# Kernel tuning notes

Measured on AMD Instinct MI355X. Metric: run time of the kernel, lower is better.

The kernel has to match this reference:

```python
import jax, jax.numpy as jnp
import numpy as np

B, T, N, F_IN, F_OUT = 8, 16, 512, 128, 64
NEG_INF = -9e15


def setup_inputs() -> dict:
    key = jax.random.key(0)
    k1, k2, k3, k4, k5 = jax.random.split(key, 5)
    x = jax.random.normal(k1, (B, T, N, F_IN), dtype=jnp.float32)
    # nn.Linear weights: FC_W [out, in], FC_a [1, 2*out], no bias
    W = jax.random.normal(k2, (F_OUT, F_IN), dtype=jnp.float32) * 0.05
    a = jax.random.normal(k3, (1, 2 * F_OUT), dtype=jnp.float32) * 0.05
    adj = jax.random.randint(k4, (N, N), 0, 2, dtype=jnp.int32)
    adj_we = jax.random.uniform(k5, (N, N), dtype=jnp.float32)
    return {"x": x, "W": W, "a": a, "adj": adj, "adj_we": adj_we}


def reference(x, W, a, adj, adj_we):
    fout = W.shape[0]
    # h = FC_W(input): [B,T,N,Fout]
    h = jnp.einsum("btnf,of->btno", x, W)
    # Additive GAT score decomposition: e[i,j] = LeakyReLU(a1.h_i + a2.h_j)
    # (equivalent to FC_a(cat([h_i, h_j])) without materializing [B,T,N,N,2F])
    a1 = a[0, :fout]
    a2 = a[0, fout:]
    src = jnp.einsum("btno,o->btn", h, a1)  # contribution of node i (repeated rows)
    dst = jnp.einsum("btno,o->btn", h, a2)  # contribution of node j (tiled rows)
    e = jax.nn.leaky_relu(src[..., :, None] + dst[..., None, :], negative_slope=0.01)
    # mask where adj <= 0, scale by edge weights, softmax over neighbors (dim=3)
    att = jnp.where(adj > 0, e, NEG_INF)
    att = att * adj_we
    att = jax.nn.softmax(att, axis=-1)
    # h_prime = attention @ h : [B,T,N,N] @ [B,T,N,Fout]
    return jnp.einsum("btij,btjo->btio", att, h)
```

## Files before the change

### kernel.cpp

```cpp
#include <hip/hip_runtime.h>
#include <hip/hip_bf16.h>

#define BTOT 128
#define NN   512
#define FIN  128
#define FOUT 64

typedef __attribute__((ext_vector_type(8))) short bf16x8;
typedef __attribute__((ext_vector_type(4))) float f32x4;

static __device__ inline ushort f2bf(float f) {
    __hip_bfloat16 h = __float2bfloat16(f);
    return *(ushort*)&h;
}
static __device__ inline float bf2f(ushort u) {
    uint v = (uint)u << 16;
    return __uint_as_float(v);
}

__global__ void k_prep(const float* __restrict__ W, const int* __restrict__ adj,
                       const float* __restrict__ we, ushort* __restrict__ Whi,
                       ushort* __restrict__ Wlo, ushort* __restrict__ cds) {
    int b = blockIdx.x;
    if (b >= 256) {
        int i = (b - 256) * 256 + threadIdx.x;
        float w = W[i];
        ushort hi = f2bf(w);
        Whi[i] = hi;
        Wlo[i] = f2bf(w - bf2f(hi));
        return;
    }
    int i = (b * 256 + threadIdx.x) * 4;
    int4   a4 = *(const int4*)&adj[i];
    float4 w4 = *(const float4*)&we[i];
    ushort o[4];
#pragma unroll
    for (int e = 0; e < 4; ++e) {
        bool  cn = ((const int*)&a4)[e] > 0;
        float w  = ((const float*)&w4)[e];
        if (cn) {
            uint ub = __float_as_uint(w * 1.44269504f);
            uint t  = ub + 0xFFFFu + ((ub >> 17) & 1u);
            o[e] = (ushort)(((t >> 17) << 1) | 1u);
        } else {
            o[e] = (w > 0.f) ? (ushort)0 : (ushort)1;
        }
    }
    *(uint2*)&cds[i] = *(uint2*)&o[0];
}

__global__ void k_feat(const float* __restrict__ x, const ushort* __restrict__ Whi,
                       const ushort* __restrict__ Wlo, const float* __restrict__ a,
                       ushort* __restrict__ ht, float* __restrict__ srcv,
                       float* __restrict__ dstv) {
    const int t    = threadIdx.x;
    const int bid  = blockIdx.x;
    const int bt   = bid & 127;
    const int nt   = bid >> 7;
    const int wv   = t >> 6, lane = t & 63;
    const int r    = lane & 15;
    const int kc   = lane >> 4;
    const int n0   = nt * 64 + wv * 16;

    const float* xrow = x + ((long)bt * NN + n0 + r) * FIN;

    f32x4 acc[4] = {{0,0,0,0},{0,0,0,0},{0,0,0,0},{0,0,0,0}};

#pragma unroll
    for (int ks = 0; ks < 4; ++ks) {
        f32x4 xa = __builtin_nontemporal_load((const f32x4*)&xrow[ks * 32 + kc * 8]);
        f32x4 xb = __builtin_nontemporal_load((const f32x4*)&xrow[ks * 32 + kc * 8 + 4]);
        float xv[8] = {xa[0], xa[1], xa[2], xa[3], xb[0], xb[1], xb[2], xb[3]};
        bf16x8 Ahi, Alo;
#pragma unroll
        for (int e = 0; e < 8; ++e) {
            uint b = __float_as_uint(xv[e]);
            float hf = __uint_as_float(b & 0xFFFF0000u);
            Ahi[e] = (short)(b >> 16);
            float rr = xv[e] - hf;
            Alo[e] = (short)(__float_as_uint(rr) >> 16);
        }
#pragma unroll
        for (int g = 0; g < 4; ++g) {
            const int wo = (g * 16 + r) * FIN + ks * 32 + kc * 8;
            bf16x8 Bhi = *(const bf16x8*)&Whi[wo];
            bf16x8 Blo = *(const bf16x8*)&Wlo[wo];
            acc[g] = __builtin_amdgcn_mfma_f32_16x16x32_bf16(Ahi, Bhi, acc[g], 0, 0, 0);
            acc[g] = __builtin_amdgcn_mfma_f32_16x16x32_bf16(Alo, Bhi, acc[g], 0, 0, 0);
            acc[g] = __builtin_amdgcn_mfma_f32_16x16x32_bf16(Ahi, Blo, acc[g], 0, 0, 0);
        }
    }

    float a1g[4], a2g[4];
#pragma unroll
    for (int g = 0; g < 4; ++g) {
        a1g[g] = a[g * 16 + r];
        a2g[g] = a[FOUT + g * 16 + r];
    }
    f32x4 s1v = {0,0,0,0}, s2v = {0,0,0,0};
#pragma unroll
    for (int g = 0; g < 4; ++g)
#pragma unroll
        for (int reg = 0; reg < 4; ++reg) {
            s1v[reg] += acc[g][reg] * a1g[g];
            s2v[reg] += acc[g][reg] * a2g[g];
        }
#pragma unroll
    for (int off = 8; off; off >>= 1)
#pragma unroll
        for (int reg = 0; reg < 4; ++reg) {
            s1v[reg] += __shfl_down(s1v[reg], off, 16);
            s2v[reg] += __shfl_down(s2v[reg], off, 16);
        }
    if (r == 0) {
        float4 o1 = make_float4(s1v[0], s1v[1], s1v[2], s1v[3]);
        float4 o2 = make_float4(s2v[0], s2v[1], s2v[2], s2v[3]);
        *(float4*)&srcv[bt * NN + n0 + kc * 4] = o1;
        *(float4*)&dstv[bt * NN + n0 + kc * 4] = o2;
    }

#pragma unroll
    for (int g = 0; g < 4; ++g) {
        uint2 pk;
        pk.x = (uint)f2bf(acc[g][0]) | ((uint)f2bf(acc[g][1]) << 16);
        pk.y = (uint)f2bf(acc[g][2]) | ((uint)f2bf(acc[g][3]) << 16);
        *(uint2*)&ht[(long)bt * (FOUT * NN) + (g * 16 + r) * NN + n0 + kc * 4] = pk;
    }
}

static __device__ inline bf16x8 make_afrag(uint4 c, float4 d0, float4 d1, float si) {
    float dv[8] = {d0.x, d0.y, d0.z, d0.w, d1.x, d1.y, d1.z, d1.w};
    uint  cw[4] = {c.x, c.y, c.z, c.w};
    bf16x8 A;
#pragma unroll
    for (int q = 0; q < 4; ++q) {
        uint u = cw[q];
        float c0 = __uint_as_float((u << 16) & 0xFFFE0000u);
        float c1 = __uint_as_float(u & 0xFFFE0000u);
        float s0 = si + dv[2 * q],     lr0 = fmaxf(s0, 0.01f * s0);
        float s1 = si + dv[2 * q + 1], lr1 = fmaxf(s1, 0.01f * s1);
        float p0 = __builtin_amdgcn_exp2f(c0 * lr0);
        float p1 = __builtin_amdgcn_exp2f(c1 * lr1);
        p0 = (u & 1u)       ? p0 : 0.f;
        p1 = (u & 0x10000u) ? p1 : 0.f;
        A[2 * q]     = (short)(__float_as_uint(p0) >> 16);
        A[2 * q + 1] = (short)(__float_as_uint(p1) >> 16);
    }
    return A;
}

__global__ __launch_bounds__(256, 4)
void k_attn(const ushort* __restrict__ ht, const float* __restrict__ srcv,
            const float* __restrict__ dstv, const ushort* __restrict__ cds,
            float* __restrict__ out) {
    __shared__ ushort hs[64 * 256];
    __shared__ float dst_s[NN];

    const int t    = threadIdx.x;
    const int bid  = blockIdx.x;
    const int bt   = bid & 127;
    const int i0   = (bid >> 7) << 6;
    const int lane = t & 63;
    const int wv   = t >> 6;
    const int r16  = lane & 15;
    const int kq   = lane >> 4;
    const int koff = kq * 8;
    const int xr   = r16 & 7;

    const int ri = i0 + wv * 16 + r16;
    const float si = srcv[bt * NN + ri];
    const ushort* cdr = cds + ri * NN;
    const ushort* htb = ht + (long)bt * (FOUT * NN);

    for (int q = t; q < NN; q += 256) dst_s[q] = dstv[bt * NN + q];

    f32x4 acc0 = {0,0,0,0}, acc1 = {0,0,0,0}, acc2 = {0,0,0,0},
          acc3 = {0,0,0,0}, accd = {0,0,0,0};
    bf16x8 ones;
#pragma unroll
    for (int j = 0; j < 8; ++j) ones[j] = (short)0x3F80;

    for (int half = 0; half < 2; ++half) {
        __syncthreads();
#pragma unroll
        for (int q = 0; q < 8; ++q) {
            int idx = q * 256 + t;
            int o = idx >> 5, c8 = idx & 31;
            float4 v = *(const float4*)&htb[(o << 9) + (half << 8) + (c8 << 3)];
            *(float4*)&hs[(o << 8) + ((c8 ^ (o & 7)) << 3)] = v;
        }
        __syncthreads();

        const int jg = half * 256;
        uint4 cA = *(const uint4*)&cdr[jg + koff];
        uint4 cB = *(const uint4*)&cdr[jg + 32 + koff];

#pragma unroll
        for (int jtl = 0; jtl < 4; ++jtl) {
            const int jgc = jg + jtl * 64;
            uint4 nA = {0,0,0,0}, nB = {0,0,0,0};
            if (jtl < 3) {
                nA = *(const uint4*)&cdr[jgc + 64 + koff];
                nB = *(const uint4*)&cdr[jgc + 96 + koff];
            }
            float4 d00 = *(float4*)&dst_s[jgc + koff];
            float4 d01 = *(float4*)&dst_s[jgc + koff + 4];
            float4 d10 = *(float4*)&dst_s[jgc + 32 + koff];
            float4 d11 = *(float4*)&dst_s[jgc + 32 + koff + 4];

            bf16x8 A0 = make_afrag(cA, d00, d01, si);
            bf16x8 A1 = make_afrag(cB, d10, d11, si);

#pragma unroll
            for (int s2 = 0; s2 < 2; ++s2) {
                bf16x8 A = s2 ? A1 : A0;
                const int c8v = jtl * 8 + s2 * 4 + kq;
                const int cs  = (c8v ^ xr) << 3;
                bf16x8 b0 = *(bf16x8*)&hs[(( 0 + r16) << 8) + cs];
                bf16x8 b1 = *(bf16x8*)&hs[((16 + r16) << 8) + cs];
                bf16x8 b2 = *(bf16x8*)&hs[((32 + r16) << 8) + cs];
                bf16x8 b3 = *(bf16x8*)&hs[((48 + r16) << 8) + cs];
                acc0 = __builtin_amdgcn_mfma_f32_16x16x32_bf16(A, b0, acc0, 0, 0, 0);
                acc1 = __builtin_amdgcn_mfma_f32_16x16x32_bf16(A, b1, acc1, 0, 0, 0);
                acc2 = __builtin_amdgcn_mfma_f32_16x16x32_bf16(A, b2, acc2, 0, 0, 0);
                acc3 = __builtin_amdgcn_mfma_f32_16x16x32_bf16(A, b3, acc3, 0, 0, 0);
                accd = __builtin_amdgcn_mfma_f32_16x16x32_bf16(A, ones, accd, 0, 0, 0);
            }
            cA = nA; cB = nB;
        }
    }

    const int orow = wv * 16 + (lane >> 4) * 4;
    const int ocol = lane & 15;
    float* ob = out + ((long)bt * NN + i0) * FOUT;
#pragma unroll
    for (int reg = 0; reg < 4; ++reg) {
        float inv = 1.0f / accd[reg];
        __builtin_nontemporal_store(acc0[reg] * inv, &ob[(orow + reg) * FOUT +  0 + ocol]);
        __builtin_nontemporal_store(acc1[reg] * inv, &ob[(orow + reg) * FOUT + 16 + ocol]);
        __builtin_nontemporal_store(acc2[reg] * inv, &ob[(orow + reg) * FOUT + 32 + ocol]);
        __builtin_nontemporal_store(acc3[reg] * inv, &ob[(orow + reg) * FOUT + 48 + ocol]);
    }
}

extern "C" void kernel_launch(void* const* d_in, const int* in_sizes, int n_in,
                              void* d_out, int out_size, void* d_ws, size_t ws_size,
                              hipStream_t stream) {
    const float* x      = (const float*)d_in[0];
    const float* W      = (const float*)d_in[1];
    const float* a      = (const float*)d_in[2];
    const int*   adj    = (const int*)d_in[3];
    const float* adj_we = (const float*)d_in[4];
    float* out = (float*)d_out;

    ushort* Whi  = (ushort*)d_ws;
    ushort* Wlo  = Whi + FOUT * FIN;
    ushort* ht   = Wlo + FOUT * FIN;
    float*  srcv = (float*)(ht + BTOT * FOUT * NN);
    float*  dstv = srcv + BTOT * NN;
    ushort* cdsw = (ushort*)(dstv + BTOT * NN);

    hipLaunchKernelGGL(k_prep, dim3(288), dim3(256), 0, stream,
                       W, adj, adj_we, Whi, Wlo, cdsw);
    hipLaunchKernelGGL(k_feat, dim3(1024), dim3(256), 0, stream,
                       x, Whi, Wlo, a, ht, srcv, dstv);
    hipLaunchKernelGGL(k_attn, dim3(1024), dim3(256), 0, stream,
                       ht, srcv, dstv, cdsw, out);
}
```

Measured before the change: 48.22 us.

## Fuse feature projection and attention into a single kernel with LDS-resident h

Merges the feature GEMM kernel and the attention kernel into one k_gat kernel. Each 512-thread block recomputes the whole projected h for one (b,t) slice directly into LDS, plus the src/dst scores, then handles attention for half of that slice's rows. This removes the global write and re-read of the bf16 h tensor and the src/dst vectors, and drops one kernel launch. Each wave now processes two 16-row tiles that share the same B fragments. In exchange, the x projection is computed twice per slice, x is read twice, and the grid shrinks to 256 large blocks using about 68KB of LDS each, which lowers occupancy.

```diff
diff --git a/kernel.cpp b/kernel.cpp
--- a/kernel.cpp
+++ b/kernel.cpp
@@ -40,92 +40,13 @@
         float w  = ((const float*)&w4)[e];
         if (cn) {
             uint ub = __float_as_uint(w * 1.44269504f);
-            uint t  = ub + 0xFFFFu + ((ub >> 17) & 1u);
-            o[e] = (ushort)(((t >> 17) << 1) | 1u);
+            uint tt = ub + 0xFFFFu + ((ub >> 17) & 1u);
+            o[e] = (ushort)(((tt >> 17) << 1) | 1u);
         } else {
             o[e] = (w > 0.f) ? (ushort)0 : (ushort)1;
         }
     }
     *(uint2*)&cds[i] = *(uint2*)&o[0];
-}
-
-__global__ void k_feat(const float* __restrict__ x, const ushort* __restrict__ Whi,
-                       const ushort* __restrict__ Wlo, const float* __restrict__ a,
-                       ushort* __restrict__ ht, float* __restrict__ srcv,
-                       float* __restrict__ dstv) {
-    const int t    = threadIdx.x;
-    const int bid  = blockIdx.x;
-    const int bt   = bid & 127;
-    const int nt   = bid >> 7;
-    const int wv   = t >> 6, lane = t & 63;
-    const int r    = lane & 15;
-    const int kc   = lane >> 4;
-    const int n0   = nt * 64 + wv * 16;
-
-    const float* xrow = x + ((long)bt * NN + n0 + r) * FIN;
-
-    f32x4 acc[4] = {{0,0,0,0},{0,0,0,0},{0,0,0,0},{0,0,0,0}};
-
-#pragma unroll
-    for (int ks = 0; ks < 4; ++ks) {
-        f32x4 xa = __builtin_nontemporal_load((const f32x4*)&xrow[ks * 32 + kc * 8]);
-        f32x4 xb = __builtin_nontemporal_load((const f32x4*)&xrow[ks * 32 + kc * 8 + 4]);
-        float xv[8] = {xa[0], xa[1], xa[2], xa[3], xb[0], xb[1], xb[2], xb[3]};
-        bf16x8 Ahi, Alo;
-#pragma unroll
-        for (int e = 0; e < 8; ++e) {
-            uint b = __float_as_uint(xv[e]);
-            float hf = __uint_as_float(b & 0xFFFF0000u);
-            Ahi[e] = (short)(b >> 16);
-            float rr = xv[e] - hf;
-            Alo[e] = (short)(__float_as_uint(rr) >> 16);
-        }
-#pragma unroll
-        for (int g = 0; g < 4; ++g) {
-            const int wo = (g * 16 + r) * FIN + ks * 32 + kc * 8;
-            bf16x8 Bhi = *(const bf16x8*)&Whi[wo];
-            bf16x8 Blo = *(const bf16x8*)&Wlo[wo];
-            acc[g] = __builtin_amdgcn_mfma_f32_16x16x32_bf16(Ahi, Bhi, acc[g], 0, 0, 0);
-            acc[g] = __builtin_amdgcn_mfma_f32_16x16x32_bf16(Alo, Bhi, acc[g], 0, 0, 0);
-            acc[g] = __builtin_amdgcn_mfma_f32_16x16x32_bf16(Ahi, Blo, acc[g], 0, 0, 0);
-        }
-    }
-
-    float a1g[4], a2g[4];
-#pragma unroll
-    for (int g = 0; g < 4; ++g) {
-        a1g[g] = a[g * 16 + r];
-        a2g[g] = a[FOUT + g * 16 + r];
-    }
-    f32x4 s1v = {0,0,0,0}, s2v = {0,0,0,0};
-#pragma unroll
-    for (int g = 0; g < 4; ++g)
-#pragma unroll
-        for (int reg = 0; reg < 4; ++reg) {
-            s1v[reg] += acc[g][reg] * a1g[g];
-            s2v[reg] += acc[g][reg] * a2g[g];
-        }
-#pragma unroll
-    for (int off = 8; off; off >>= 1)
-#pragma unroll
-        for (int reg = 0; reg < 4; ++reg) {
-            s1v[reg] += __shfl_down(s1v[reg], off, 16);
-            s2v[reg] += __shfl_down(s2v[reg], off, 16);
-        }
-    if (r == 0) {
-        float4 o1 = make_float4(s1v[0], s1v[1], s1v[2], s1v[3]);
-        float4 o2 = make_float4(s2v[0], s2v[1], s2v[2], s2v[3]);
-        *(float4*)&srcv[bt * NN + n0 + kc * 4] = o1;
-        *(float4*)&dstv[bt * NN + n0 + kc * 4] = o2;
-    }
-
-#pragma unroll
-    for (int g = 0; g < 4; ++g) {
-        uint2 pk;
-        pk.x = (uint)f2bf(acc[g][0]) | ((uint)f2bf(acc[g][1]) << 16);
-        pk.y = (uint)f2bf(acc[g][2]) | ((uint)f2bf(acc[g][3]) << 16);
-        *(uint2*)&ht[(long)bt * (FOUT * NN) + (g * 16 + r) * NN + n0 + kc * 4] = pk;
-    }
 }
 
 static __device__ inline bf16x8 make_afrag(uint4 c, float4 d0, float4 d1, float si) {
@@ -149,97 +70,173 @@
     return A;
 }
 
-__global__ __launch_bounds__(256, 4)
-void k_attn(const ushort* __restrict__ ht, const float* __restrict__ srcv,
-            const float* __restrict__ dstv, const ushort* __restrict__ cds,
-            float* __restrict__ out) {
-    __shared__ ushort hs[64 * 256];
+__global__ __launch_bounds__(512, 2)
+void k_gat(const float* __restrict__ x, const ushort* __restrict__ Whi,
+           const ushort* __restrict__ Wlo, const float* __restrict__ av,
+           const ushort* __restrict__ cds, float* __restrict__ out) {
+    __shared__ ushort hs[FOUT * NN];
+    __shared__ float src_s[NN];
     __shared__ float dst_s[NN];
 
     const int t    = threadIdx.x;
     const int bid  = blockIdx.x;
     const int bt   = bid & 127;
-    const int i0   = (bid >> 7) << 6;
+    const int hv   = bid >> 7;
+    const int wv   = t >> 6;
     const int lane = t & 63;
-    const int wv   = t >> 6;
     const int r16  = lane & 15;
-    const int kq   = lane >> 4;
-    const int koff = kq * 8;
+    const int kc   = lane >> 4;
     const int xr   = r16 & 7;
 
-    const int ri = i0 + wv * 16 + r16;
-    const float si = srcv[bt * NN + ri];
-    const ushort* cdr = cds + ri * NN;
-    const ushort* htb = ht + (long)bt * (FOUT * NN);
-
-    for (int q = t; q < NN; q += 256) dst_s[q] = dstv[bt * NN + q];
-
-    f32x4 acc0 = {0,0,0,0}, acc1 = {0,0,0,0}, acc2 = {0,0,0,0},
-          acc3 = {0,0,0,0}, accd = {0,0,0,0};
+    float a1g[4], a2g[4];
+#pragma unroll
+    for (int g = 0; g < 4; ++g) {
+        a1g[g] = av[g * 16 + r16];
+        a2g[g] = av[FOUT + g * 16 + r16];
+    }
+
+#pragma unroll
+    for (int p = 0; p < 4; ++p) {
+        const int n0 = wv * 64 + p * 16;
+        const float* xrow = x + ((long)bt * NN + n0 + r16) * FIN;
+        f32x4 acc[4] = {{0,0,0,0},{0,0,0,0},{0,0,0,0},{0,0,0,0}};
+#pragma unroll
+        for (int ks = 0; ks < 4; ++ks) {
+            float4 xa = *(const float4*)&xrow[ks * 32 + kc * 8];
+            float4 xb = *(const float4*)&xrow[ks * 32 + kc * 8 + 4];
+            float xv[8] = {xa.x, xa.y, xa.z, xa.w, xb.x, xb.y, xb.z, xb.w};
+            bf16x8 Ahi, Alo;
+#pragma unroll
+            for (int e = 0; e < 8; ++e) {
+                uint b = __float_as_uint(xv[e]);
+                Ahi[e] = (short)(b >> 16);
+                float rr = xv[e] - __uint_as_float(b & 0xFFFF0000u);
+                Alo[e] = (short)(__float_as_uint(rr) >> 16);
+            }
+#pragma unroll
+            for (int g = 0; g < 4; ++g) {
+                const int wo = (g * 16 + r16) * FIN + ks * 32 + kc * 8;
+                bf16x8 Bhi = *(const bf16x8*)&Whi[wo];
+                bf16x8 Blo = *(const bf16x8*)&Wlo[wo];
+                acc[g] = __builtin_amdgcn_mfma_f32_16x16x32_bf16(Ahi, Bhi, acc[g], 0, 0, 0);
+                acc[g] = __builtin_amdgcn_mfma_f32_16x16x32_bf16(Alo, Bhi, acc[g], 0, 0, 0);
+                acc[g] = __builtin_amdgcn_mfma_f32_16x16x32_bf16(Ahi, Blo, acc[g], 0, 0, 0);
+            }
+        }
+        f32x4 s1v = {0,0,0,0}, s2v = {0,0,0,0};
+#pragma unroll
+        for (int g = 0; g < 4; ++g)
+#pragma unroll
+            for (int reg = 0; reg < 4; ++reg) {
+                s1v[reg] += acc[g][reg] * a1g[g];
+                s2v[reg] += acc[g][reg] * a2g[g];
+            }
+#pragma unroll
+        for (int off = 8; off; off >>= 1)
+#pragma unroll
+            for (int reg = 0; reg < 4; ++reg) {
+                s1v[reg] += __shfl_down(s1v[reg], off, 16);
+                s2v[reg] += __shfl_down(s2v[reg], off, 16);
+            }
+        if (r16 == 0) {
+            *(float4*)&src_s[n0 + kc * 4] = make_float4(s1v[0], s1v[1], s1v[2], s1v[3]);
+            *(float4*)&dst_s[n0 + kc * 4] = make_float4(s2v[0], s2v[1], s2v[2], s2v[3]);
+        }
+#pragma unroll
+        for (int g = 0; g < 4; ++g) {
+            uint2 pk;
+            pk.x = (uint)f2bf(acc[g][0]) | ((uint)f2bf(acc[g][1]) << 16);
+            pk.y = (uint)f2bf(acc[g][2]) | ((uint)f2bf(acc[g][3]) << 16);
+            const int o  = g * 16 + r16;
+            const int j0 = n0 + kc * 4;
+            *(uint2*)&hs[o * NN + ((((j0 >> 3) ^ (o & 7)) << 3) | (j0 & 7))] = pk;
+        }
+    }
+    __syncthreads();
+
+    const int i0   = (hv * 4 + (wv >> 1)) * 64;
+    const int sub  = wv & 1;
+    const int koff = kc * 8;
+
+    const int ri0 = i0 + sub * 32 + r16;
+    const int ri1 = ri0 + 16;
+    const float si0 = src_s[ri0];
+    const float si1 = src_s[ri1];
+    const ushort* cdr0 = cds + ri0 * NN;
+    const ushort* cdr1 = cds + ri1 * NN;
+
+    f32x4 p0c0 = {0,0,0,0}, p0c1 = {0,0,0,0}, p0c2 = {0,0,0,0}, p0c3 = {0,0,0,0},
+          p0d  = {0,0,0,0};
+    f32x4 p1c0 = {0,0,0,0}, p1c1 = {0,0,0,0}, p1c2 = {0,0,0,0}, p1c3 = {0,0,0,0},
+          p1d  = {0,0,0,0};
     bf16x8 ones;
 #pragma unroll
     for (int j = 0; j < 8; ++j) ones[j] = (short)0x3F80;
 
-    for (int half = 0; half < 2; ++half) {
-        __syncthreads();
-#pragma unroll
-        for (int q = 0; q < 8; ++q) {
-            int idx = q * 256 + t;
-            int o = idx >> 5, c8 = idx & 31;
-            float4 v = *(const float4*)&htb[(o << 9) + (half << 8) + (c8 << 3)];
-            *(float4*)&hs[(o << 8) + ((c8 ^ (o & 7)) << 3)] = v;
-        }
-        __syncthreads();
-
-        const int jg = half * 256;
-        uint4 cA = *(const uint4*)&cdr[jg + koff];
-        uint4 cB = *(const uint4*)&cdr[jg + 32 + koff];
-
-#pragma unroll
-        for (int jtl = 0; jtl < 4; ++jtl) {
-            const int jgc = jg + jtl * 64;
-            uint4 nA = {0,0,0,0}, nB = {0,0,0,0};
-            if (jtl < 3) {
-                nA = *(const uint4*)&cdr[jgc + 64 + koff];
-                nB = *(const uint4*)&cdr[jgc + 96 + koff];
-            }
-            float4 d00 = *(float4*)&dst_s[jgc + koff];
-            float4 d01 = *(float4*)&dst_s[jgc + koff + 4];
-            float4 d10 = *(float4*)&dst_s[jgc + 32 + koff];
-            float4 d11 = *(float4*)&dst_s[jgc + 32 + koff + 4];
-
-            bf16x8 A0 = make_afrag(cA, d00, d01, si);
-            bf16x8 A1 = make_afrag(cB, d10, d11, si);
-
-#pragma unroll
-            for (int s2 = 0; s2 < 2; ++s2) {
-                bf16x8 A = s2 ? A1 : A0;
-                const int c8v = jtl * 8 + s2 * 4 + kq;
-                const int cs  = (c8v ^ xr) << 3;
-                bf16x8 b0 = *(bf16x8*)&hs[(( 0 + r16) << 8) + cs];
-                bf16x8 b1 = *(bf16x8*)&hs[((16 + r16) << 8) + cs];
-                bf16x8 b2 = *(bf16x8*)&hs[((32 + r16) << 8) + cs];
-                bf16x8 b3 = *(bf16x8*)&hs[((48 + r16) << 8) + cs];
-                acc0 = __builtin_amdgcn_mfma_f32_16x16x32_bf16(A, b0, acc0, 0, 0, 0);
-                acc1 = __builtin_amdgcn_mfma_f32_16x16x32_bf16(A, b1, acc1, 0, 0, 0);
-                acc2 = __builtin_amdgcn_mfma_f32_16x16x32_bf16(A, b2, acc2, 0, 0, 0);
-                acc3 = __builtin_amdgcn_mfma_f32_16x16x32_bf16(A, b3, acc3, 0, 0, 0);
-                accd = __builtin_amdgcn_mfma_f32_16x16x32_bf16(A, ones, accd, 0, 0, 0);
-            }
-            cA = nA; cB = nB;
-        }
-    }
-
-    const int orow = wv * 16 + (lane >> 4) * 4;
-    const int ocol = lane & 15;
-    float* ob = out + ((long)bt * NN + i0) * FOUT;
+    uint4 fA0 = *(const uint4*)&cdr0[koff];
+    uint4 fB0 = *(const uint4*)&cdr0[32 + koff];
+    uint4 fA1 = *(const uint4*)&cdr1[koff];
+    uint4 fB1 = *(const uint4*)&cdr1[32 + koff];
+
+#pragma unroll
+    for (int ch = 0; ch < 8; ++ch) {
+        const int j0 = ch * 64;
+        uint4 cA0 = fA0, cB0 = fB0, cA1 = fA1, cB1 = fB1;
+        if (ch < 7) {
+            fA0 = *(const uint4*)&cdr0[j0 + 64 + koff];
+            fB0 = *(const uint4*)&cdr0[j0 + 96 + koff];
+            fA1 = *(const uint4*)&cdr1[j0 + 64 + koff];
+            fB1 = *(const uint4*)&cdr1[j0 + 96 + koff];
+        }
+        float4 d00 = *(float4*)&dst_s[j0 + koff];
+        float4 d01 = *(float4*)&dst_s[j0 + koff + 4];
+        float4 d10 = *(float4*)&dst_s[j0 + 32 + koff];
+        float4 d11 = *(float4*)&dst_s[j0 + 32 + koff + 4];
+
+        bf16x8 A00 = make_afrag(cA0, d00, d01, si0);
+        bf16x8 A01 = make_afrag(cB0, d10, d11, si0);
+        bf16x8 A10 = make_afrag(cA1, d00, d01, si1);
+        bf16x8 A11 = make_afrag(cB1, d10, d11, si1);
+
+#pragma unroll
+        for (int s2 = 0; s2 < 2; ++s2) {
+            const int c8v = ch * 8 + s2 * 4 + kc;
+            const int cs  = (c8v ^ xr) << 3;
+            bf16x8 b0 = *(bf16x8*)&hs[(( 0 + r16) * NN) + cs];
+            bf16x8 b1 = *(bf16x8*)&hs[((16 + r16) * NN) + cs];
+            bf16x8 b2 = *(bf16x8*)&hs[((32 + r16) * NN) + cs];
+            bf16x8 b3 = *(bf16x8*)&hs[((48 + r16) * NN) + cs];
+            bf16x8 A0 = s2 ? A01 : A00;
+            bf16x8 A1 = s2 ? A11 : A10;
+            p0c0 = __builtin_amdgcn_mfma_f32_16x16x32_bf16(A0, b0, p0c0, 0, 0, 0);
+            p0c1 = __builtin_amdgcn_mfma_f32_16x16x32_bf16(A0, b1, p0c1, 0, 0, 0);
+            p0c2 = __builtin_amdgcn_mfma_f32_16x16x32_bf16(A0, b2, p0c2, 0, 0, 0);
+            p0c3 = __builtin_amdgcn_mfma_f32_16x16x32_bf16(A0, b3, p0c3, 0, 0, 0);
+            p0d  = __builtin_amdgcn_mfma_f32_16x16x32_bf16(A0, ones, p0d, 0, 0, 0);
+            p1c0 = __builtin_amdgcn_mfma_f32_16x16x32_bf16(A1, b0, p1c0, 0, 0, 0);
+            p1c1 = __builtin_amdgcn_mfma_f32_16x16x32_bf16(A1, b1, p1c1, 0, 0, 0);
+            p1c2 = __builtin_amdgcn_mfma_f32_16x16x32_bf16(A1, b2, p1c2, 0, 0, 0);
+            p1c3 = __builtin_amdgcn_mfma_f32_16x16x32_bf16(A1, b3, p1c3, 0, 0, 0);
+            p1d  = __builtin_amdgcn_mfma_f32_16x16x32_bf16(A1, ones, p1d, 0, 0, 0);
+        }
+    }
+
+    const int orow = kc * 4;
+    float* ob0 = out + ((long)bt * NN + i0 + sub * 32) * FOUT;
+    float* ob1 = ob0 + 16 * FOUT;
 #pragma unroll
     for (int reg = 0; reg < 4; ++reg) {
-        float inv = 1.0f / accd[reg];
-        __builtin_nontemporal_store(acc0[reg] * inv, &ob[(orow + reg) * FOUT +  0 + ocol]);
-        __builtin_nontemporal_store(acc1[reg] * inv, &ob[(orow + reg) * FOUT + 16 + ocol]);
-        __builtin_nontemporal_store(acc2[reg] * inv, &ob[(orow + reg) * FOUT + 32 + ocol]);
-        __builtin_nontemporal_store(acc3[reg] * inv, &ob[(orow + reg) * FOUT + 48 + ocol]);
+        float inv0 = 1.0f / p0d[reg];
+        float inv1 = 1.0f / p1d[reg];
+        const int rw = (orow + reg) * FOUT + r16;
+        __builtin_nontemporal_store(p0c0[reg] * inv0, &ob0[rw +  0]);
+        __builtin_nontemporal_store(p0c1[reg] * inv0, &ob0[rw + 16]);
+        __builtin_nontemporal_store(p0c2[reg] * inv0, &ob0[rw + 32]);
+        __builtin_nontemporal_store(p0c3[reg] * inv0, &ob0[rw + 48]);
+        __builtin_nontemporal_store(p1c0[reg] * inv1, &ob1[rw +  0]);
+        __builtin_nontemporal_store(p1c1[reg] * inv1, &ob1[rw + 16]);
+        __builtin_nontemporal_store(p1c2[reg] * inv1, &ob1[rw + 32]);
+        __builtin_nontemporal_store(p1c3[reg] * inv1, &ob1[rw + 48]);
     }
 }
 
@@ -255,15 +252,10 @@
 
     ushort* Whi  = (ushort*)d_ws;
     ushort* Wlo  = Whi + FOUT * FIN;
-    ushort* ht   = Wlo + FOUT * FIN;
-    float*  srcv = (float*)(ht + BTOT * FOUT * NN);
-    float*  dstv = srcv + BTOT * NN;
-    ushort* cdsw = (ushort*)(dstv + BTOT * NN);
+    ushort* cdsw = Wlo + FOUT * FIN;
 
     hipLaunchKernelGGL(k_prep, dim3(288), dim3(256), 0, stream,
                        W, adj, adj_we, Whi, Wlo, cdsw);
-    hipLaunchKernelGGL(k_feat, dim3(1024), dim3(256), 0, stream,
-                       x, Whi, Wlo, a, ht, srcv, dstv);
-    hipLaunchKernelGGL(k_attn, dim3(1024), dim3(256), 0, stream,
-                       ht, srcv, dstv, cdsw, out);
-}
+    hipLaunchKernelGGL(k_gat, dim3(256), dim3(512), 0, stream,
+                       x, Whi, Wlo, a, cdsw, out);
+}
```

Result: slower. 61.64 us (+27.8%).

## Process two 16-row tiles per wave in attention kernel to reuse B fragments

Applied to the files above, without the earlier changes.

Each wave in k_attn now handles 32 query rows (two 16-row MFMA tiles) instead of 16, so each block covers 128 rows and the grid halves to 512 blocks. Every h tile staged in shared memory and every B fragment read from LDS now feeds twice as many MFMAs, which cuts LDS reads and global reloads of h per output row. The adjacency-code prefetch for the first chunk of each half is also moved ahead of the shared-memory staging barrier. The cost is doubled accumulator registers, which may lower occupancy, and fewer blocks spread across the CUs.

```diff
diff --git a/kernel.cpp b/kernel.cpp
--- a/kernel.cpp
+++ b/kernel.cpp
@@ -40,8 +40,8 @@
         float w  = ((const float*)&w4)[e];
         if (cn) {
             uint ub = __float_as_uint(w * 1.44269504f);
-            uint t  = ub + 0xFFFFu + ((ub >> 17) & 1u);
-            o[e] = (ushort)(((t >> 17) << 1) | 1u);
+            uint tt = ub + 0xFFFFu + ((ub >> 17) & 1u);
+            o[e] = (ushort)(((tt >> 17) << 1) | 1u);
         } else {
             o[e] = (w > 0.f) ? (ushort)0 : (ushort)1;
         }
@@ -159,28 +159,39 @@
     const int t    = threadIdx.x;
     const int bid  = blockIdx.x;
     const int bt   = bid & 127;
-    const int i0   = (bid >> 7) << 6;
+    const int q4   = bid >> 7;
     const int lane = t & 63;
     const int wv   = t >> 6;
     const int r16  = lane & 15;
-    const int kq   = lane >> 4;
-    const int koff = kq * 8;
+    const int kc   = lane >> 4;
+    const int koff = kc * 8;
     const int xr   = r16 & 7;
 
-    const int ri = i0 + wv * 16 + r16;
-    const float si = srcv[bt * NN + ri];
-    const ushort* cdr = cds + ri * NN;
-    const ushort* htb = ht + (long)bt * (FOUT * NN);
+    const int ri0 = q4 * 128 + wv * 32 + r16;
+    const int ri1 = ri0 + 16;
+    const float si0 = srcv[bt * NN + ri0];
+    const float si1 = srcv[bt * NN + ri1];
+    const ushort* cdr0 = cds + ri0 * NN;
+    const ushort* cdr1 = cds + ri1 * NN;
+    const ushort* htb  = ht + (long)bt * (FOUT * NN);
 
     for (int q = t; q < NN; q += 256) dst_s[q] = dstv[bt * NN + q];
 
-    f32x4 acc0 = {0,0,0,0}, acc1 = {0,0,0,0}, acc2 = {0,0,0,0},
-          acc3 = {0,0,0,0}, accd = {0,0,0,0};
+    f32x4 a0c0 = {0,0,0,0}, a0c1 = {0,0,0,0}, a0c2 = {0,0,0,0}, a0c3 = {0,0,0,0},
+          a0d  = {0,0,0,0};
+    f32x4 a1c0 = {0,0,0,0}, a1c1 = {0,0,0,0}, a1c2 = {0,0,0,0}, a1c3 = {0,0,0,0},
+          a1d  = {0,0,0,0};
     bf16x8 ones;
 #pragma unroll
     for (int j = 0; j < 8; ++j) ones[j] = (short)0x3F80;
 
     for (int half = 0; half < 2; ++half) {
+        const int jg = half * 256;
+        uint4 fA0 = *(const uint4*)&cdr0[jg + koff];
+        uint4 fB0 = *(const uint4*)&cdr0[jg + 32 + koff];
+        uint4 fA1 = *(const uint4*)&cdr1[jg + koff];
+        uint4 fB1 = *(const uint4*)&cdr1[jg + 32 + koff];
+
         __syncthreads();
 #pragma unroll
         for (int q = 0; q < 8; ++q) {
@@ -191,55 +202,67 @@
         }
         __syncthreads();
 
-        const int jg = half * 256;
-        uint4 cA = *(const uint4*)&cdr[jg + koff];
-        uint4 cB = *(const uint4*)&cdr[jg + 32 + koff];
-
 #pragma unroll
         for (int jtl = 0; jtl < 4; ++jtl) {
             const int jgc = jg + jtl * 64;
-            uint4 nA = {0,0,0,0}, nB = {0,0,0,0};
+            uint4 nA0 = {0,0,0,0}, nB0 = {0,0,0,0},
+                  nA1 = {0,0,0,0}, nB1 = {0,0,0,0};
             if (jtl < 3) {
-                nA = *(const uint4*)&cdr[jgc + 64 + koff];
-                nB = *(const uint4*)&cdr[jgc + 96 + koff];
+                nA0 = *(const uint4*)&cdr0[jgc + 64 + koff];
+                nB0 = *(const uint4*)&cdr0[jgc + 96 + koff];
+                nA1 = *(const uint4*)&cdr1[jgc + 64 + koff];
+                nB1 = *(const uint4*)&cdr1[jgc + 96 + koff];
             }
             float4 d00 = *(float4*)&dst_s[jgc + koff];
             float4 d01 = *(float4*)&dst_s[jgc + koff + 4];
             float4 d10 = *(float4*)&dst_s[jgc + 32 + koff];
             float4 d11 = *(float4*)&dst_s[jgc + 32 + koff + 4];
 
-            bf16x8 A0 = make_afrag(cA, d00, d01, si);
-            bf16x8 A1 = make_afrag(cB, d10, d11, si);
+            bf16x8 A00 = make_afrag(fA0, d00, d01, si0);
+            bf16x8 A01 = make_afrag(fB0, d10, d11, si0);
+            bf16x8 A10 = make_afrag(fA1, d00, d01, si1);
+            bf16x8 A11 = make_afrag(fB1, d10, d11, si1);
 
 #pragma unroll
             for (int s2 = 0; s2 < 2; ++s2) {
-                bf16x8 A = s2 ? A1 : A0;
-                const int c8v = jtl * 8 + s2 * 4 + kq;
+                const int c8v = jtl * 8 + s2 * 4 + kc;
                 const int cs  = (c8v ^ xr) << 3;
                 bf16x8 b0 = *(bf16x8*)&hs[(( 0 + r16) << 8) + cs];
                 bf16x8 b1 = *(bf16x8*)&hs[((16 + r16) << 8) + cs];
                 bf16x8 b2 = *(bf16x8*)&hs[((32 + r16) << 8) + cs];
                 bf16x8 b3 = *(bf16x8*)&hs[((48 + r16) << 8) + cs];
-                acc0 = __builtin_amdgcn_mfma_f32_16x16x32_bf16(A, b0, acc0, 0, 0, 0);
-                acc1 = __builtin_amdgcn_mfma_f32_16x16x32_bf16(A, b1, acc1, 0, 0, 0);
-                acc2 = __builtin_amdgcn_mfma_f32_16x16x32_bf16(A, b2, acc2, 0, 0, 0);
-                acc3 = __builtin_amdgcn_mfma_f32_16x16x32_bf16(A, b3, acc3, 0, 0, 0);
-                accd = __builtin_amdgcn_mfma_f32_16x16x32_bf16(A, ones, accd, 0, 0, 0);
+                bf16x8 A0 = s2 ? A01 : A00;
+                bf16x8 A1 = s2 ? A11 : A10;
+                a0c0 = __builtin_amdgcn_mfma_f32_16x16x32_bf16(A0, b0, a0c0, 0, 0, 0);
+                a0c1 = __builtin_amdgcn_mfma_f32_16x16x32_bf16(A0, b1, a0c1, 0, 0, 0);
+                a0c2 = __builtin_amdgcn_mfma_f32_16x16x32_bf16(A0, b2, a0c2, 0, 0, 0);
+                a0c3 = __builtin_amdgcn_mfma_f32_16x16x32_bf16(A0, b3, a0c3, 0, 0, 0);
+                a0d  = __builtin_amdgcn_mfma_f32_16x16x32_bf16(A0, ones, a0d, 0, 0, 0);
+                a1c0 = __builtin_amdgcn_mfma_f32_16x16x32_bf16(A1, b0, a1c0, 0, 0, 0);
+                a1c1 = __builtin_amdgcn_mfma_f32_16x16x32_bf16(A1, b1, a1c1, 0, 0, 0);
+                a1c2 = __builtin_amdgcn_mfma_f32_16x16x32_bf16(A1, b2, a1c2, 0, 0, 0);
+                a1c3 = __builtin_amdgcn_mfma_f32_16x16x32_bf16(A1, b3, a1c3, 0, 0, 0);
+                a1d  = __builtin_amdgcn_mfma_f32_16x16x32_bf16(A1, ones, a1d, 0, 0, 0);
             }
-            cA = nA; cB = nB;
-        }
-    }
-
-    const int orow = wv * 16 + (lane >> 4) * 4;
-    const int ocol = lane & 15;
-    float* ob = out + ((long)bt * NN + i0) * FOUT;
+            fA0 = nA0; fB0 = nB0; fA1 = nA1; fB1 = nB1;
+        }
+    }
+
+    float* ob0 = out + ((long)bt * NN + q4 * 128 + wv * 32) * FOUT;
+    float* ob1 = ob0 + 16 * FOUT;
 #pragma unroll
     for (int reg = 0; reg < 4; ++reg) {
-        float inv = 1.0f / accd[reg];
-        __builtin_nontemporal_store(acc0[reg] * inv, &ob[(orow + reg) * FOUT +  0 + ocol]);
-        __builtin_nontemporal_store(acc1[reg] * inv, &ob[(orow + reg) * FOUT + 16 + ocol]);
-        __builtin_nontemporal_store(acc2[reg] * inv, &ob[(orow + reg) * FOUT + 32 + ocol]);
-        __builtin_nontemporal_store(acc3[reg] * inv, &ob[(orow + reg) * FOUT + 48 + ocol]);
+        float inv0 = 1.0f / a0d[reg];
+        float inv1 = 1.0f / a1d[reg];
+        const int rw = (kc * 4 + reg) * FOUT + r16;
+        __builtin_nontemporal_store(a0c0[reg] * inv0, &ob0[rw +  0]);
+        __builtin_nontemporal_store(a0c1[reg] * inv0, &ob0[rw + 16]);
+        __builtin_nontemporal_store(a0c2[reg] * inv0, &ob0[rw + 32]);
+        __builtin_nontemporal_store(a0c3[reg] * inv0, &ob0[rw + 48]);
+        __builtin_nontemporal_store(a1c0[reg] * inv1, &ob1[rw +  0]);
+        __builtin_nontemporal_store(a1c1[reg] * inv1, &ob1[rw + 16]);
+        __builtin_nontemporal_store(a1c2[reg] * inv1, &ob1[rw + 32]);
+        __builtin_nontemporal_store(a1c3[reg] * inv1, &ob1[rw + 48]);
     }
 }
 
@@ -264,6 +287,6 @@
                        W, adj, adj_we, Whi, Wlo, cdsw);
     hipLaunchKernelGGL(k_feat, dim3(1024), dim3(256), 0, stream,
                        x, Whi, Wlo, a, ht, srcv, dstv);
-    hipLaunchKernelGGL(k_attn, dim3(1024), dim3(256), 0, stream,
+    hipLaunchKernelGGL(k_attn, dim3(512), dim3(256), 0, stream,
                        ht, srcv, dstv, cdsw, out);
 }
```

Result: slower. 54.57 us (+13.1%).
